# Kernel tuning notes

Measured on AMD Instinct MI355X. Metric: run time of the kernel, lower is better.

Reference implementation:

```python
import jax, jax.numpy as jnp
import numpy as np

B, T, U, H = 16, 256, 96, 512


def setup_inputs() -> dict:
    key = jax.random.key(0)
    k1, k2, k3, k4 = jax.random.split(key, 4)
    f = jax.random.normal(k1, (B, T, H), dtype=jnp.float32)
    g = jax.random.normal(k2, (B, U, H), dtype=jnp.float32)
    f_len = jax.random.randint(k3, (B,), 1, T + 1, dtype=jnp.int32)
    g_len = jax.random.randint(k4, (B,), 1, U + 1, dtype=jnp.int32)
    return {"f": f, "g": g, "f_len": f_len, "g_len": g_len}


def reference(f, g, f_len, g_len):
    # f: (B, T, H), g: (B, U, H) -> h: (B, T, U, H)
    # h[b,t,u,:] = f[b,t,:] + g[b,u,:] for t < f_len[b], u < g_len[b]; else 0.
    Bc, Tc, Hc = f.shape
    Uc = g.shape[1]
    t_valid = jnp.arange(Tc)[None, :] < f_len[:, None]          # (B, T)
    u_valid = jnp.arange(Uc)[None, :] < g_len[:, None]          # (B, U)
    mask = (t_valid[:, :, None] & u_valid[:, None, :])[..., None]  # (B, T, U, 1)
    h = f[:, :, None, :] + g[:, None, :, :]                     # (B, T, U, H)
    return jnp.where(mask, h, jnp.zeros((), dtype=f.dtype))
```

## Files before the change

kernel.cpp:

```cpp
#include <hip/hip_runtime.h>
#include <hip/hip_bf16.h>


#define TJ_B 16
#define TJ_T 256
#define TJ_U 96
#define TJ_H 512
#define TJ_H4 (TJ_H / 4)

__global__ __launch_bounds__(TJ_H4) void TransducerJoint_66915590472509_kernel(
    const float4* __restrict__ f,
    const float4* __restrict__ g,
    const int* __restrict__ f_len,
    const int* __restrict__ g_len,
    float4* __restrict__ out)
{
    const int bid = blockIdx.x;
    const int u  = bid % TJ_U;
    const int bt = bid / TJ_U;
    const int t  = bt % TJ_T;
    const int b  = bt / TJ_T;
    const int h4 = threadIdx.x;

    const bool valid = (t < f_len[b]) && (u < g_len[b]);

    float4 res;
    if (valid) {
        const float4 fv = f[(size_t)(b * TJ_T + t) * TJ_H4 + h4];
        const float4 gv = g[(size_t)(b * TJ_U + u) * TJ_H4 + h4];
        res = make_float4(fv.x + gv.x, fv.y + gv.y, fv.z + gv.z, fv.w + gv.w);
    } else {
        res = make_float4(0.f, 0.f, 0.f, 0.f);
    }
    out[(size_t)bid * TJ_H4 + h4] = res;
}

extern "C" void kernel_launch(void* const* d_in, const int* in_sizes, int n_in,
                              void* d_out, int out_size, void* d_ws, size_t ws_size,
                              hipStream_t stream) {
    const float4* f     = (const float4*)d_in[0];
    const float4* g     = (const float4*)d_in[1];
    const int*    f_len = (const int*)d_in[2];
    const int*    g_len = (const int*)d_in[3];
    float4*       out   = (float4*)d_out;

    const int nblocks = TJ_B * TJ_T * TJ_U;
    TransducerJoint_66915590472509_kernel<<<nblocks, TJ_H4, 0, stream>>>(
        f, g, f_len, g_len, out);
}
```

Before: 780.2 us.

## Process one (b,t) row per block looping over u with nontemporal stores

Restructures the grid so each 256-thread block handles one (b,t) pair, loading the f row once and iterating over all u positions in two interleaved halves. This replaces hundreds of thousands of tiny blocks with a few thousand, reducing launch and scheduling overhead and redundant f reads. Output writes use nontemporal stores to avoid polluting caches with the large write-only tensor. The block count is now smaller, which could limit latency hiding.

```diff
diff --git a/kernel.cpp b/kernel.cpp
--- a/kernel.cpp
+++ b/kernel.cpp
@@ -8,43 +8,53 @@
 #define TJ_H 512
 #define TJ_H4 (TJ_H / 4)
 
-__global__ __launch_bounds__(TJ_H4) void TransducerJoint_66915590472509_kernel(
-    const float4* __restrict__ f,
-    const float4* __restrict__ g,
+typedef float fx4 __attribute__((ext_vector_type(4)));
+
+__global__ __launch_bounds__(256) void TransducerJoint_66915590472509_kernel(
+    const fx4* __restrict__ f,
+    const fx4* __restrict__ g,
     const int* __restrict__ f_len,
     const int* __restrict__ g_len,
-    float4* __restrict__ out)
+    fx4* __restrict__ out)
 {
-    const int bid = blockIdx.x;
-    const int u  = bid % TJ_U;
-    const int bt = bid / TJ_U;
-    const int t  = bt % TJ_T;
-    const int b  = bt / TJ_T;
-    const int h4 = threadIdx.x;
+    const int bt = blockIdx.x;
+    const int b  = bt >> 8;
+    const int t  = bt & 255;
 
-    const bool valid = (t < f_len[b]) && (u < g_len[b]);
+    const int h4    = threadIdx.x & (TJ_H4 - 1);
+    const int uhalf = threadIdx.x >> 7;
 
-    float4 res;
-    if (valid) {
-        const float4 fv = f[(size_t)(b * TJ_T + t) * TJ_H4 + h4];
-        const float4 gv = g[(size_t)(b * TJ_U + u) * TJ_H4 + h4];
-        res = make_float4(fv.x + gv.x, fv.y + gv.y, fv.z + gv.z, fv.w + gv.w);
-    } else {
-        res = make_float4(0.f, 0.f, 0.f, 0.f);
+    const int flen = f_len[b];
+    const int glen = g_len[b];
+    const bool tvalid = (t < flen);
+
+    fx4 fv = (fx4)0.f;
+    if (tvalid) fv = f[(size_t)bt * TJ_H4 + h4];
+
+    const fx4* gp = g + ((size_t)(b * TJ_U + uhalf)) * TJ_H4 + h4;
+    fx4* op = out + ((size_t)bt * TJ_U + uhalf) * TJ_H4 + h4;
+
+    #pragma unroll 8
+    for (int u = uhalf; u < TJ_U; u += 2) {
+        const fx4 gv = *gp;
+        const bool ok = tvalid && (u < glen);
+        fx4 r = ok ? (fv + gv) : (fx4)0.f;
+        __builtin_nontemporal_store(r, op);
+        gp += 2 * TJ_H4;
+        op += 2 * TJ_H4;
     }
-    out[(size_t)bid * TJ_H4 + h4] = res;
 }
 
 extern "C" void kernel_launch(void* const* d_in, const int* in_sizes, int n_in,
                               void* d_out, int out_size, void* d_ws, size_t ws_size,
                               hipStream_t stream) {
-    const float4* f     = (const float4*)d_in[0];
-    const float4* g     = (const float4*)d_in[1];
-    const int*    f_len = (const int*)d_in[2];
-    const int*    g_len = (const int*)d_in[3];
-    float4*       out   = (float4*)d_out;
+    const fx4* f     = (const fx4*)d_in[0];
+    const fx4* g     = (const fx4*)d_in[1];
+    const int* f_len = (const int*)d_in[2];
+    const int* g_len = (const int*)d_in[3];
+    fx4*       out   = (fx4*)d_out;
 
-    const int nblocks = TJ_B * TJ_T * TJ_U;
-    TransducerJoint_66915590472509_kernel<<<nblocks, TJ_H4, 0, stream>>>(
+    const int nblocks = TJ_B * TJ_T;
+    TransducerJoint_66915590472509_kernel<<<nblocks, 256, 0, stream>>>(
         f, g, f_len, g_len, out);
 }
```

Result: slower. 806.0 us (+3.3%).
